# Kernel tuning notes

Hardware: AMD Instinct MI355X
Metric: run time of the kernel (lower is better)

The kernel has to match this reference:

```python
import jax, jax.numpy as jnp
import numpy as np

N_NODES = 100000


def _gcn_conv(x, W, b, row, col, norm, n):
    # PyG GCNConv: h = x @ W, then symmetric-normalized scatter-add, then bias
    h = x @ W                          # [N, out]
    msg = h[col] * norm[:, None]       # gather at source nodes, scale per-edge
    out = jax.ops.segment_sum(msg, row, num_segments=n)  # scatter-add to dest
    return out + b


def setup_inputs() -> dict:
    key = jax.random.key(0)
    k1, k2, k3, k4, k5, k6 = jax.random.split(key, 6)
    F_in, H, C = 128, 128, 64
    E = 1600000
    x = jax.random.normal(k1, (N_NODES, F_in), dtype=jnp.float32)
    edge_index = jax.random.randint(k2, (2, E), 0, N_NODES, dtype=jnp.int64)
    s1 = 1.0 / np.sqrt(F_in)
    s2 = 1.0 / np.sqrt(H)
    W1 = jax.random.uniform(k3, (F_in, H), jnp.float32, -s1, s1)
    b1 = jax.random.uniform(k4, (H,), jnp.float32, -s1, s1)
    W2 = jax.random.uniform(k5, (H, C), jnp.float32, -s2, s2)
    b2 = jax.random.uniform(k6, (C,), jnp.float32, -s2, s2)
    return {"x": x, "edge_index": edge_index, "W1": W1, "b1": b1, "W2": W2, "b2": b2}


def reference(x, edge_index, W1, b1, W2, b2):
    n = x.shape[0]
    # add self-loops (GCNConv default)
    loops = jnp.arange(n, dtype=edge_index.dtype)
    row = jnp.concatenate([edge_index[0], loops])  # destination
    col = jnp.concatenate([edge_index[1], loops])  # source
    # symmetric normalization deg^{-1/2}[row] * deg^{-1/2}[col]
    deg = jax.ops.segment_sum(jnp.ones_like(row, dtype=x.dtype), row, num_segments=n)
    dinv = jnp.where(deg > 0, jax.lax.rsqrt(deg), 0.0)
    norm = dinv[row] * dinv[col]       # [E+N]
    h = jax.nn.relu(_gcn_conv(x, W1, b1, row, col, norm, n))
    # dropout is identity in eval mode
    out = _gcn_conv(h, W2, b2, row, col, norm, n)
    return jax.nn.log_softmax(out, axis=1)
```

## Files before the change

### kernel.cpp

```cpp
#include <hip/hip_runtime.h>
#include <hip/hip_fp16.h>
#include <cstdint>
#include <cstddef>

#define TPB 256
#define CAP 64
#define FWSHIFT 9
#define FWROWS 512
#define CAPB 96
#define DEC_ITERS 32


using half8 = __attribute__((ext_vector_type(8))) _Float16;
using f32x4 = __attribute__((ext_vector_type(4))) float;

__global__ void k_setup(const void* __restrict__ ei, int E, int N,
                        const float* __restrict__ W1, const float* __restrict__ W2,
                        _Float16* __restrict__ wf1, _Float16* __restrict__ wf2,
                        int2* __restrict__ bpairs, int* __restrict__ bcnt,
                        int nDec, int nFW) {
    int b = blockIdx.x;
    if (b < 16) {
        int i = b * TPB + threadIdx.x;
        int k  = i >> 5;
        int n0 = (i & 31) * 4;
        float4 w = ((const float4*)W1)[i];
        int ct = n0 >> 4, kb = k >> 5;
        int lane0 = ((k >> 3) & 3) * 16 + (n0 & 15);
        int j = k & 7;
        int base = ((ct * 4 + kb) * 64 + lane0) * 8 + j;
        wf1[base]      = (_Float16)w.x;
        wf1[base + 8]  = (_Float16)w.y;
        wf1[base + 16] = (_Float16)w.z;
        wf1[base + 24] = (_Float16)w.w;
    } else if (b < 24) {
        int i = (b - 16) * TPB + threadIdx.x;
        int k  = i >> 4;
        int n0 = (i & 15) * 4;
        float4 w = ((const float4*)W2)[i];
        int ct = n0 >> 4, kb = k >> 5;
        int lane0 = ((k >> 3) & 3) * 16 + (n0 & 15);
        int j = k & 7;
        int base = ((ct * 4 + kb) * 64 + lane0) * 8 + j;
        wf2[base]      = (_Float16)w.x;
        wf2[base + 8]  = (_Float16)w.y;
        wf2[base + 16] = (_Float16)w.z;
        wf2[base + 24] = (_Float16)w.w;
    } else {
        const int dblk = b - 24;
        const int tid  = threadIdx.x;
        __shared__ int bad;
        __shared__ int cur[256];
        if (tid == 0) bad = 0;
        for (int f = tid; f < nFW; f += TPB) cur[f] = 0;
        __syncthreads();
        if (tid < 256) {
            long long v = ((const long long*)ei)[tid];
            if (v < 0 || v >= (long long)N) bad = 1;
        }
        __syncthreads();
        const int is64 = !bad;
        const int base = dblk * (TPB * DEC_ITERS);
        const long long* e64 = (const long long*)ei;
        const int* e32 = (const int*)ei;

        for (int it = 0; it < DEC_ITERS; it += 4) {
            int d[4], s[4]; bool val[4];
#pragma unroll
            for (int k = 0; k < 4; ++k) {
                int e = base + (it + k) * TPB + tid;
                val[k] = e < E;
                if (val[k]) {
                    if (is64) { d[k] = (int)e64[e]; s[k] = (int)e64[(long long)E + e]; }
                    else      { d[k] = e32[e];      s[k] = e32[E + e]; }
                }
            }
#pragma unroll
            for (int k = 0; k < 4; ++k) {
                if (val[k]) {
                    int fw  = d[k] >> FWSHIFT;
                    int pos = atomicAdd(&cur[fw], 1);
                    if (pos < CAPB)
                        bpairs[((size_t)fw * nDec + dblk) * CAPB + pos] =
                            make_int2(d[k], s[k]);
                }
            }
        }
        __syncthreads();
        for (int f = tid; f < nFW; f += TPB) {
            int c = cur[f];
            bcnt[(size_t)f * nDec + dblk] = c > CAPB ? CAPB : c;
        }
    }
}

__global__ __launch_bounds__(256)
void k_mega(const int2* __restrict__ bpairs, const int* __restrict__ bcnt,
            int nDec, int N,
            int* __restrict__ cnt, float* __restrict__ dinv,
            int* __restrict__ slots,
            const float* __restrict__ x, const half8* __restrict__ wf1,
            __half* __restrict__ xw1, int nFW, int nGemm) {
    __shared__ __align__(16) _Float16 Of[4][16 * 136];
    __shared__ int cur[FWROWS];
    __shared__ int sc[256];
    __shared__ int excl[257];

    const int tid = threadIdx.x;

    if ((int)blockIdx.x < nFW) {
        const int fw = blockIdx.x;
        for (int i = tid; i < FWROWS; i += TPB) cur[i] = 0;
        int c = (tid < nDec) ? bcnt[(size_t)fw * nDec + tid] : 0;
        sc[tid] = c;
        __syncthreads();
        for (int off = 1; off < 256; off <<= 1) {
            int v = (tid >= off) ? sc[tid - off] : 0;
            __syncthreads();
            sc[tid] += v;
            __syncthreads();
        }
        if (tid == 0) excl[0] = 0;
        excl[tid + 1] = sc[tid];
        __syncthreads();
        const int total = excl[nDec];

        for (int i = tid; i < total; i += TPB) {
            int lo = 0, hi = nDec;
            while (hi - lo > 1) {
                int mid = (lo + hi) >> 1;
                if (excl[mid] <= i) lo = mid; else hi = mid;
            }
            int2 p = bpairs[((size_t)fw * nDec + lo) * CAPB + (i - excl[lo])];
            int pos = atomicAdd(&cur[p.x - (fw << FWSHIFT)], 1);
            if (pos < CAP)
                slots[(size_t)p.x * CAP + pos] = p.y;
        }
        __syncthreads();
        for (int i = tid; i < FWROWS; i += TPB) {
            int node = (fw << FWSHIFT) + i;
            if (node < N) {
                int cc = cur[i];
                cnt[node]  = cc;
                dinv[node] = rsqrtf((float)cc + 1.0f);
            }
        }
    } else {
        const int gb = (int)blockIdx.x - nFW;
        const int wave = tid >> 6, lane = tid & 63;
        const int m = lane & 15, quad = lane >> 4;
        const int nRowTiles = (N + 15) >> 4;

        for (int rt = gb * 4 + wave; rt < nRowTiles; rt += nGemm * 4) {
            const int row0 = rt * 16;
            const int arow = row0 + m;
            const bool rvalid = arow < N;
            const float* xrow = x + (size_t)(rvalid ? arow : 0) * 128;

            f32x4 acc[8];
#pragma unroll
            for (int ct = 0; ct < 8; ++ct) acc[ct] = (f32x4){0.f, 0.f, 0.f, 0.f};

#pragma unroll
            for (int kb = 0; kb < 4; ++kb) {
                const float4* ap = (const float4*)(xrow + kb * 32 + quad * 8);
                float4 a0 = ap[0], a1 = ap[1];
                half8 a;
                a[0] = (_Float16)a0.x; a[1] = (_Float16)a0.y;
                a[2] = (_Float16)a0.z; a[3] = (_Float16)a0.w;
                a[4] = (_Float16)a1.x; a[5] = (_Float16)a1.y;
                a[6] = (_Float16)a1.z; a[7] = (_Float16)a1.w;
#pragma unroll
                for (int ct = 0; ct < 8; ++ct) {
                    half8 bfr = wf1[(ct * 4 + kb) * 64 + lane];
                    acc[ct] = __builtin_amdgcn_mfma_f32_16x16x32_f16(a, bfr, acc[ct], 0, 0, 0);
                }
            }

            _Float16* myO = &Of[wave][0];
#pragma unroll
            for (int ct = 0; ct < 8; ++ct)
#pragma unroll
                for (int r = 0; r < 4; ++r)
                    myO[(quad * 4 + r) * 136 + ct * 16 + m] = (_Float16)acc[ct][r];
            int vr = N - row0; if (vr > 16) vr = 16;
            float4* dst = (float4*)(xw1 + (size_t)row0 * 128);
            for (int i = lane; i < vr * 16; i += 64) {
                int r = i >> 4, q = i & 15;
                dst[r * 16 + q] = *(const float4*)&myO[r * 136 + q * 8];
            }
        }
    }
}

__global__ __launch_bounds__(256)
void k_g1g2(const __half* __restrict__ xw1, const int* __restrict__ cnt,
            const float* __restrict__ dinv,
            const int* __restrict__ slots, const float* __restrict__ bias,
            const half8* __restrict__ wf2, __half* __restrict__ xw2, int N) {
    __shared__ __align__(16) _Float16 Ht[16 * 136];
    __shared__ __align__(16) _Float16 Of[16 * 72];
    __shared__ float dv16[16];

    const int row0 = blockIdx.x * 16;
    const int local = threadIdx.x >> 4;
    const int lane16 = threadIdx.x & 15;
    const int node = row0 + local;

    {
        union { __half2 h2[4]; float4 f; } u;
        float dvn = 0.f;
        if (node < N) {
            int cn = cnt[node];
            int len = cn > CAP ? CAP : cn;
            dvn = dinv[node];
            const int* sl = slots + (size_t)node * CAP;
            float acc[8];
            {
                float4 raw = *(const float4*)(xw1 + (size_t)node * 128 + lane16 * 8);
                const __half2* hp = (const __half2*)&raw;
#pragma unroll
                for (int k = 0; k < 4; ++k) {
                    float2 f = __half22float2(hp[k]);
                    acc[2 * k] = dvn * f.x; acc[2 * k + 1] = dvn * f.y;
                }
            }
            int j = 0;
            for (; j + 3 < len; j += 4) {
                int4 cc = *(const int4*)(sl + j);
                float dv0 = dinv[cc.x];
                float dv1 = dinv[cc.y];
                float dv2 = dinv[cc.z];
                float dv3 = dinv[cc.w];
                float4 raw0 = *(const float4*)(xw1 + (size_t)cc.x * 128 + lane16 * 8);
                float4 raw1 = *(const float4*)(xw1 + (size_t)cc.y * 128 + lane16 * 8);
                float4 raw2 = *(const float4*)(xw1 + (size_t)cc.z * 128 + lane16 * 8);
                float4 raw3 = *(const float4*)(xw1 + (size_t)cc.w * 128 + lane16 * 8);
                const __half2* h0 = (const __half2*)&raw0;
                const __half2* h1 = (const __half2*)&raw1;
                const __half2* h2 = (const __half2*)&raw2;
                const __half2* h3 = (const __half2*)&raw3;
#pragma unroll
                for (int k = 0; k < 4; ++k) {
                    float2 f0 = __half22float2(h0[k]);
                    float2 f1 = __half22float2(h1[k]);
                    float2 f2 = __half22float2(h2[k]);
                    float2 f3 = __half22float2(h3[k]);
                    acc[2 * k]     = fmaf(dv0, f0.x, fmaf(dv1, f1.x,
                                     fmaf(dv2, f2.x, fmaf(dv3, f3.x, acc[2 * k]))));
                    acc[2 * k + 1] = fmaf(dv0, f0.y, fmaf(dv1, f1.y,
                                     fmaf(dv2, f2.y, fmaf(dv3, f3.y, acc[2 * k + 1]))));
                }
            }
            for (; j < len; ++j) {
                int c = sl[j];
                float dv = dinv[c];
                float4 raw = *(const float4*)(xw1 + (size_t)c * 128 + lane16 * 8);
                const __half2* hp = (const __half2*)&raw;
#pragma unroll
                for (int k = 0; k < 4; ++k) {
                    float2 f = __half22float2(hp[k]);
                    acc[2 * k]     = fmaf(dv, f.x, acc[2 * k]);
                    acc[2 * k + 1] = fmaf(dv, f.y, acc[2 * k + 1]);
                }
            }
            float4 b01 = ((const float4*)bias)[lane16 * 2];
            float4 b23 = ((const float4*)bias)[lane16 * 2 + 1];
            float v[8];
            v[0] = b01.x + dvn * acc[0]; v[1] = b01.y + dvn * acc[1];
            v[2] = b01.z + dvn * acc[2]; v[3] = b01.w + dvn * acc[3];
            v[4] = b23.x + dvn * acc[4]; v[5] = b23.y + dvn * acc[5];
            v[6] = b23.z + dvn * acc[6]; v[7] = b23.w + dvn * acc[7];
#pragma unroll
            for (int k = 0; k < 4; ++k)
                u.h2[k] = __floats2half2_rn(fmaxf(v[2 * k], 0.f), fmaxf(v[2 * k + 1], 0.f));
        } else {
            u.f = make_float4(0.f, 0.f, 0.f, 0.f);
        }
        if (lane16 == 0) dv16[local] = dvn;
        *(float4*)(Ht + local * 136 + lane16 * 8) = u.f;
    }
    __syncthreads();

    {
        const int wave = threadIdx.x >> 6, lane = threadIdx.x & 63;
        const int m = lane & 15, quad = lane >> 4;
        f32x4 acc = (f32x4){0.f, 0.f, 0.f, 0.f};
#pragma unroll
        for (int kb = 0; kb < 4; ++kb) {
            half8 a = *(const half8*)(Ht + m * 136 + kb * 32 + quad * 8);
            half8 b = wf2[(wave * 4 + kb) * 64 + lane];
            acc = __builtin_amdgcn_mfma_f32_16x16x32_f16(a, b, acc, 0, 0, 0);
        }
#pragma unroll
        for (int r = 0; r < 4; ++r)
            Of[(quad * 4 + r) * 72 + wave * 16 + m] =
                (_Float16)(acc[r] * dv16[quad * 4 + r]);
    }
    __syncthreads();
    {
        int vr = N - row0; if (vr > 16) vr = 16;
        float4* dst = (float4*)(xw2 + (size_t)row0 * 64);
        for (int i = threadIdx.x; i < vr * 8; i += TPB) {
            int r = i >> 3, q = i & 7;
            dst[r * 8 + q] = *(const float4*)&Of[r * 72 + q * 8];
        }
    }
}

__global__ void k_gather2_lsm(const __half* __restrict__ xws, const int* __restrict__ cnt,
                              const float* __restrict__ dinv,
                              const int* __restrict__ slots,
                              const float* __restrict__ bias, float* __restrict__ out, int N) {
    long long t = (long long)blockIdx.x * TPB + threadIdx.x;
    int node = (int)(t >> 4);
    int lane = (int)(t & 15);
    if (node >= N) return;
    int cn = cnt[node];
    int len = cn > CAP ? CAP : cn;
    float dvn = dinv[node];
    const int* sl = slots + (size_t)node * CAP;
    float a0, a1, a2, a3;
    {
        float2 raw = *(const float2*)(xws + (size_t)node * 64 + lane * 4);
        const __half2* hp = (const __half2*)&raw;
        float2 f0 = __half22float2(hp[0]), f1 = __half22float2(hp[1]);
        a0 = f0.x; a1 = f0.y; a2 = f1.x; a3 = f1.y;
    }
    int j = 0;
    for (; j + 3 < len; j += 4) {
        int4 cc = *(const int4*)(sl + j);
        float2 raw0 = *(const float2*)(xws + (size_t)cc.x * 64 + lane * 4);
        float2 raw1 = *(const float2*)(xws + (size_t)cc.y * 64 + lane * 4);
        float2 raw2 = *(const float2*)(xws + (size_t)cc.z * 64 + lane * 4);
        float2 raw3 = *(const float2*)(xws + (size_t)cc.w * 64 + lane * 4);
        const __half2* h0 = (const __half2*)&raw0;
        const __half2* h1 = (const __half2*)&raw1;
        const __half2* h2 = (const __half2*)&raw2;
        const __half2* h3 = (const __half2*)&raw3;
        float2 f00 = __half22float2(h0[0]), f01 = __half22float2(h0[1]);
        float2 f10 = __half22float2(h1[0]), f11 = __half22float2(h1[1]);
        float2 f20 = __half22float2(h2[0]), f21 = __half22float2(h2[1]);
        float2 f30 = __half22float2(h3[0]), f31 = __half22float2(h3[1]);
        a0 += (f00.x + f10.x) + (f20.x + f30.x);
        a1 += (f00.y + f10.y) + (f20.y + f30.y);
        a2 += (f01.x + f11.x) + (f21.x + f31.x);
        a3 += (f01.y + f11.y) + (f21.y + f31.y);
    }
    for (; j < len; ++j) {
        int c = sl[j];
        float2 raw = *(const float2*)(xws + (size_t)c * 64 + lane * 4);
        const __half2* hp = (const __half2*)&raw;
        float2 f0 = __half22float2(hp[0]), f1 = __half22float2(hp[1]);
        a0 += f0.x; a1 += f0.y; a2 += f1.x; a3 += f1.y;
    }
    float4 bb = ((const float4*)bias)[lane];
    float v0 = bb.x + dvn * a0, v1 = bb.y + dvn * a1;
    float v2 = bb.z + dvn * a2, v3 = bb.w + dvn * a3;

    float m = fmaxf(fmaxf(v0, v1), fmaxf(v2, v3));
#pragma unroll
    for (int off = 1; off < 16; off <<= 1) m = fmaxf(m, __shfl_xor(m, off));
    float s = expf(v0 - m) + expf(v1 - m) + expf(v2 - m) + expf(v3 - m);
#pragma unroll
    for (int off = 1; off < 16; off <<= 1) s += __shfl_xor(s, off);
    float ls = m + logf(s);
    ((float4*)(out + (size_t)node * 64))[lane] =
        make_float4(v0 - ls, v1 - ls, v2 - ls, v3 - ls);
}

extern "C" void kernel_launch(void* const* d_in, const int* in_sizes, int n_in,
                              void* d_out, int out_size, void* d_ws, size_t ws_size,
                              hipStream_t stream) {
    const float* x  = (const float*)d_in[0];
    const void*  ei = d_in[1];
    const float* W1 = (const float*)d_in[2];
    const float* b1 = (const float*)d_in[3];
    const float* W2 = (const float*)d_in[4];
    const float* b2 = (const float*)d_in[5];
    float* out = (float*)d_out;

    const int N = in_sizes[0] / 128;
    const int E = in_sizes[1] / 2;

    const int nFW  = (N + FWROWS - 1) >> FWSHIFT;
    const int nDec = (E + TPB * DEC_ITERS - 1) / (TPB * DEC_ITERS);

    char* base = (char*)d_ws;
    size_t off = 0;
    auto alloc = [&](size_t bytes) { char* p = base + off; off = (off + bytes + 255) & ~(size_t)255; return p; };
    int*      cnt    = (int*)alloc((size_t)N * sizeof(int));
    float*    dinv   = (float*)alloc((size_t)N * sizeof(float));
    _Float16* wf1    = (_Float16*)alloc(128 * 128 * sizeof(_Float16));
    _Float16* wf2    = (_Float16*)alloc(128 * 64 * sizeof(_Float16));
    int*      bcnt   = (int*)alloc((size_t)nFW * nDec * sizeof(int));
    int2*     bpairs = (int2*)alloc((size_t)nFW * nDec * CAPB * sizeof(int2));
    int*      slots  = (int*)alloc((size_t)N * CAP * sizeof(int));
    __half*   xw1    = (__half*)alloc((size_t)N * 128 * sizeof(__half));
    __half*   xw2    = (__half*)alloc((size_t)N * 64 * sizeof(__half));
    (void)ws_size;

    const int nGemm = 512;
    const int nodeTiles = (N + 15) / 16;

    k_setup<<<24 + nDec, TPB, 0, stream>>>(ei, E, N, W1, W2, wf1, wf2,
                                           bpairs, bcnt, nDec, nFW);

    k_mega<<<nFW + nGemm, TPB, 0, stream>>>(bpairs, bcnt, nDec, N, cnt, dinv,
                                            slots, x, (const half8*)wf1, xw1,
                                            nFW, nGemm);

    k_g1g2<<<nodeTiles, TPB, 0, stream>>>(xw1, cnt, dinv, slots, b1,
                                          (const half8*)wf2, xw2, N);

    {
        long long t = (long long)N * 16;
        k_gather2_lsm<<<(int)((t + TPB - 1) / TPB), TPB, 0, stream>>>(xw2, cnt, dinv, slots, b2, out, N);
    }
}
```

Before: 257.7 us.

## Move X@W1 GEMM into setup kernel, split slot fill, unroll gathers by 8

The dense X@W1 GEMM moves out of the mega kernel into the edge-decode setup kernel. Each GEMM block converts W1 into fp16 MFMA fragments in shared memory instead of reading a prepacked global buffer. Slot filling becomes its own kernel that walks each decode bucket sequentially with vector loads, replacing the prefix-scan plus binary-search indexing. Both gather kernels gain an 8-wide unrolled loop to keep more independent loads in flight. The cost is that every GEMM block redoes the W1 conversion, and the setup kernel's shared-memory footprint and register pressure grow.

```diff
diff --git a/kernel.cpp b/kernel.cpp
--- a/kernel.cpp
+++ b/kernel.cpp
@@ -14,27 +14,26 @@
 using half8 = __attribute__((ext_vector_type(8))) _Float16;
 using f32x4 = __attribute__((ext_vector_type(4))) float;
 
-__global__ void k_setup(const void* __restrict__ ei, int E, int N,
-                        const float* __restrict__ W1, const float* __restrict__ W2,
-                        _Float16* __restrict__ wf1, _Float16* __restrict__ wf2,
-                        int2* __restrict__ bpairs, int* __restrict__ bcnt,
-                        int nDec, int nFW) {
-    int b = blockIdx.x;
-    if (b < 16) {
-        int i = b * TPB + threadIdx.x;
-        int k  = i >> 5;
-        int n0 = (i & 31) * 4;
-        float4 w = ((const float4*)W1)[i];
-        int ct = n0 >> 4, kb = k >> 5;
-        int lane0 = ((k >> 3) & 3) * 16 + (n0 & 15);
-        int j = k & 7;
-        int base = ((ct * 4 + kb) * 64 + lane0) * 8 + j;
-        wf1[base]      = (_Float16)w.x;
-        wf1[base + 8]  = (_Float16)w.y;
-        wf1[base + 16] = (_Float16)w.z;
-        wf1[base + 24] = (_Float16)w.w;
-    } else if (b < 24) {
-        int i = (b - 16) * TPB + threadIdx.x;
+struct GemmSm {
+    _Float16 Wl[32 * 64 * 8];
+    _Float16 Of[4][16 * 136];
+};
+struct DecSm { int cur[256]; int bad; };
+union SetupSm { GemmSm g; DecSm d; };
+
+__global__ __launch_bounds__(256)
+void k_setup(const void* __restrict__ ei, int E, int N,
+             const float* __restrict__ W1, const float* __restrict__ W2,
+             _Float16* __restrict__ wf2,
+             int2* __restrict__ bpairs, int* __restrict__ bcnt,
+             int nDec, int nFW,
+             const float* __restrict__ x, __half* __restrict__ xw1, int nGemm) {
+    __shared__ __align__(16) SetupSm sm;
+    const int b = blockIdx.x;
+    const int tid = threadIdx.x;
+
+    if (b < 8) {
+        int i = b * TPB + tid;
         int k  = i >> 4;
         int n0 = (i & 15) * 4;
         float4 w = ((const float4*)W2)[i];
@@ -46,20 +45,17 @@
         wf2[base + 8]  = (_Float16)w.y;
         wf2[base + 16] = (_Float16)w.z;
         wf2[base + 24] = (_Float16)w.w;
-    } else {
-        const int dblk = b - 24;
-        const int tid  = threadIdx.x;
-        __shared__ int bad;
-        __shared__ int cur[256];
-        if (tid == 0) bad = 0;
-        for (int f = tid; f < nFW; f += TPB) cur[f] = 0;
+    } else if (b < 8 + nDec) {
+        const int dblk = b - 8;
+        if (tid == 0) sm.d.bad = 0;
+        for (int f = tid; f < nFW; f += TPB) sm.d.cur[f] = 0;
         __syncthreads();
-        if (tid < 256) {
+        {
             long long v = ((const long long*)ei)[tid];
-            if (v < 0 || v >= (long long)N) bad = 1;
+            if (v < 0 || v >= (long long)N) sm.d.bad = 1;
         }
         __syncthreads();
-        const int is64 = !bad;
+        const int is64 = !sm.d.bad;
         const int base = dblk * (TPB * DEC_ITERS);
         const long long* e64 = (const long long*)ei;
         const int* e32 = (const int*)ei;
@@ -79,7 +75,7 @@
             for (int k = 0; k < 4; ++k) {
                 if (val[k]) {
                     int fw  = d[k] >> FWSHIFT;
-                    int pos = atomicAdd(&cur[fw], 1);
+                    int pos = atomicAdd(&sm.d.cur[fw], 1);
                     if (pos < CAPB)
                         bpairs[((size_t)fw * nDec + dblk) * CAPB + pos] =
                             make_int2(d[k], s[k]);
@@ -88,65 +84,26 @@
         }
         __syncthreads();
         for (int f = tid; f < nFW; f += TPB) {
-            int c = cur[f];
+            int c = sm.d.cur[f];
             bcnt[(size_t)f * nDec + dblk] = c > CAPB ? CAPB : c;
         }
-    }
-}
-
-__global__ __launch_bounds__(256)
-void k_mega(const int2* __restrict__ bpairs, const int* __restrict__ bcnt,
-            int nDec, int N,
-            int* __restrict__ cnt, float* __restrict__ dinv,
-            int* __restrict__ slots,
-            const float* __restrict__ x, const half8* __restrict__ wf1,
-            __half* __restrict__ xw1, int nFW, int nGemm) {
-    __shared__ __align__(16) _Float16 Of[4][16 * 136];
-    __shared__ int cur[FWROWS];
-    __shared__ int sc[256];
-    __shared__ int excl[257];
-
-    const int tid = threadIdx.x;
-
-    if ((int)blockIdx.x < nFW) {
-        const int fw = blockIdx.x;
-        for (int i = tid; i < FWROWS; i += TPB) cur[i] = 0;
-        int c = (tid < nDec) ? bcnt[(size_t)fw * nDec + tid] : 0;
-        sc[tid] = c;
+    } else {
+        const int gb = b - 8 - nDec;
+        for (int i = tid; i < 4096; i += TPB) {
+            float4 w = ((const float4*)W1)[i];
+            int k  = i >> 5;
+            int n0 = (i & 31) * 4;
+            int ct = n0 >> 4, kb = k >> 5;
+            int lane0 = ((k >> 3) & 3) * 16 + (n0 & 15);
+            int j = k & 7;
+            int bs = ((ct * 4 + kb) * 64 + lane0) * 8 + j;
+            sm.g.Wl[bs]      = (_Float16)w.x;
+            sm.g.Wl[bs + 8]  = (_Float16)w.y;
+            sm.g.Wl[bs + 16] = (_Float16)w.z;
+            sm.g.Wl[bs + 24] = (_Float16)w.w;
+        }
         __syncthreads();
-        for (int off = 1; off < 256; off <<= 1) {
-            int v = (tid >= off) ? sc[tid - off] : 0;
-            __syncthreads();
-            sc[tid] += v;
-            __syncthreads();
-        }
-        if (tid == 0) excl[0] = 0;
-        excl[tid + 1] = sc[tid];
-        __syncthreads();
-        const int total = excl[nDec];
-
-        for (int i = tid; i < total; i += TPB) {
-            int lo = 0, hi = nDec;
-            while (hi - lo > 1) {
-                int mid = (lo + hi) >> 1;
-                if (excl[mid] <= i) lo = mid; else hi = mid;
-            }
-            int2 p = bpairs[((size_t)fw * nDec + lo) * CAPB + (i - excl[lo])];
-            int pos = atomicAdd(&cur[p.x - (fw << FWSHIFT)], 1);
-            if (pos < CAP)
-                slots[(size_t)p.x * CAP + pos] = p.y;
-        }
-        __syncthreads();
-        for (int i = tid; i < FWROWS; i += TPB) {
-            int node = (fw << FWSHIFT) + i;
-            if (node < N) {
-                int cc = cur[i];
-                cnt[node]  = cc;
-                dinv[node] = rsqrtf((float)cc + 1.0f);
-            }
-        }
-    } else {
-        const int gb = (int)blockIdx.x - nFW;
+        const half8* wl = (const half8*)sm.g.Wl;
         const int wave = tid >> 6, lane = tid & 63;
         const int m = lane & 15, quad = lane >> 4;
         const int nRowTiles = (N + 15) >> 4;
@@ -172,12 +129,12 @@
                 a[6] = (_Float16)a1.z; a[7] = (_Float16)a1.w;
 #pragma unroll
                 for (int ct = 0; ct < 8; ++ct) {
-                    half8 bfr = wf1[(ct * 4 + kb) * 64 + lane];
+                    half8 bfr = wl[(ct * 4 + kb) * 64 + lane];
                     acc[ct] = __builtin_amdgcn_mfma_f32_16x16x32_f16(a, bfr, acc[ct], 0, 0, 0);
                 }
             }
 
-            _Float16* myO = &Of[wave][0];
+            _Float16* myO = &sm.g.Of[wave][0];
 #pragma unroll
             for (int ct = 0; ct < 8; ++ct)
 #pragma unroll
@@ -189,6 +146,53 @@
                 int r = i >> 4, q = i & 15;
                 dst[r * 16 + q] = *(const float4*)&myO[r * 136 + q * 8];
             }
+        }
+    }
+}
+
+__global__ __launch_bounds__(256)
+void k_fill(const int2* __restrict__ bpairs, const int* __restrict__ bcnt,
+            int nDec, int N,
+            int* __restrict__ cnt, float* __restrict__ dinv,
+            int* __restrict__ slots) {
+    __shared__ int cur[FWROWS];
+    const int fw = blockIdx.x;
+    const int tid = threadIdx.x;
+    const int lo = fw << FWSHIFT;
+    for (int i = tid; i < FWROWS; i += TPB) cur[i] = 0;
+    __syncthreads();
+
+    for (int s = tid; s < nDec; s += TPB) {
+        const int c = bcnt[(size_t)fw * nDec + s];
+        const int2* bp = bpairs + ((size_t)fw * nDec + s) * CAPB;
+        int j = 0;
+        for (; j + 3 < c; j += 4) {
+            const int4* q4 = (const int4*)(bp + j);
+            int4 u0 = q4[0], u1 = q4[1];
+            int2 p0 = make_int2(u0.x, u0.y), p1 = make_int2(u0.z, u0.w);
+            int2 p2 = make_int2(u1.x, u1.y), p3 = make_int2(u1.z, u1.w);
+            int q0 = atomicAdd(&cur[p0.x - lo], 1);
+            int q1 = atomicAdd(&cur[p1.x - lo], 1);
+            int q2 = atomicAdd(&cur[p2.x - lo], 1);
+            int q3 = atomicAdd(&cur[p3.x - lo], 1);
+            if (q0 < CAP) slots[(size_t)p0.x * CAP + q0] = p0.y;
+            if (q1 < CAP) slots[(size_t)p1.x * CAP + q1] = p1.y;
+            if (q2 < CAP) slots[(size_t)p2.x * CAP + q2] = p2.y;
+            if (q3 < CAP) slots[(size_t)p3.x * CAP + q3] = p3.y;
+        }
+        for (; j < c; ++j) {
+            int2 p = bp[j];
+            int pos = atomicAdd(&cur[p.x - lo], 1);
+            if (pos < CAP) slots[(size_t)p.x * CAP + pos] = p.y;
+        }
+    }
+    __syncthreads();
+    for (int i = tid; i < FWROWS; i += TPB) {
+        int node = lo + i;
+        if (node < N) {
+            int cc = cur[i];
+            cnt[node]  = cc;
+            dinv[node] = rsqrtf((float)cc + 1.0f);
         }
     }
 }
@@ -226,20 +230,59 @@
                 }
             }
             int j = 0;
+            for (; j + 7 < len; j += 8) {
+                int4 ca = *(const int4*)(sl + j);
+                int4 cb = *(const int4*)(sl + j + 4);
+                float dv0 = dinv[ca.x], dv1 = dinv[ca.y];
+                float dv2 = dinv[ca.z], dv3 = dinv[ca.w];
+                float dv4 = dinv[cb.x], dv5 = dinv[cb.y];
+                float dv6 = dinv[cb.z], dv7 = dinv[cb.w];
+                float4 r0 = *(const float4*)(xw1 + (size_t)ca.x * 128 + lane16 * 8);
+                float4 r1 = *(const float4*)(xw1 + (size_t)ca.y * 128 + lane16 * 8);
+                float4 r2 = *(const float4*)(xw1 + (size_t)ca.z * 128 + lane16 * 8);
+                float4 r3 = *(const float4*)(xw1 + (size_t)ca.w * 128 + lane16 * 8);
+                float4 r4 = *(const float4*)(xw1 + (size_t)cb.x * 128 + lane16 * 8);
+                float4 r5 = *(const float4*)(xw1 + (size_t)cb.y * 128 + lane16 * 8);
+                float4 r6 = *(const float4*)(xw1 + (size_t)cb.z * 128 + lane16 * 8);
+                float4 r7 = *(const float4*)(xw1 + (size_t)cb.w * 128 + lane16 * 8);
+                const __half2* h0 = (const __half2*)&r0;
+                const __half2* h1 = (const __half2*)&r1;
+                const __half2* h2 = (const __half2*)&r2;
+                const __half2* h3 = (const __half2*)&r3;
+                const __half2* h4 = (const __half2*)&r4;
+                const __half2* h5 = (const __half2*)&r5;
+                const __half2* h6 = (const __half2*)&r6;
+                const __half2* h7 = (const __half2*)&r7;
+#pragma unroll
+                for (int k = 0; k < 4; ++k) {
+                    float2 f0 = __half22float2(h0[k]);
+                    float2 f1 = __half22float2(h1[k]);
+                    float2 f2 = __half22float2(h2[k]);
+                    float2 f3 = __half22float2(h3[k]);
+                    float2 f4 = __half22float2(h4[k]);
+                    float2 f5 = __half22float2(h5[k]);
+                    float2 f6 = __half22float2(h6[k]);
+                    float2 f7 = __half22float2(h7[k]);
+                    float Ax = fmaf(dv0, f0.x, fmaf(dv1, f1.x, fmaf(dv2, f2.x, dv3 * f3.x)));
+                    float Bx = fmaf(dv4, f4.x, fmaf(dv5, f5.x, fmaf(dv6, f6.x, dv7 * f7.x)));
+                    float Ay = fmaf(dv0, f0.y, fmaf(dv1, f1.y, fmaf(dv2, f2.y, dv3 * f3.y)));
+                    float By = fmaf(dv4, f4.y, fmaf(dv5, f5.y, fmaf(dv6, f6.y, dv7 * f7.y)));
+                    acc[2 * k]     += Ax + Bx;
+                    acc[2 * k + 1] += Ay + By;
+                }
+            }
             for (; j + 3 < len; j += 4) {
                 int4 cc = *(const int4*)(sl + j);
-                float dv0 = dinv[cc.x];
-                float dv1 = dinv[cc.y];
-                float dv2 = dinv[cc.z];
-                float dv3 = dinv[cc.w];
-                float4 raw0 = *(const float4*)(xw1 + (size_t)cc.x * 128 + lane16 * 8);
-                float4 raw1 = *(const float4*)(xw1 + (size_t)cc.y * 128 + lane16 * 8);
-                float4 raw2 = *(const float4*)(xw1 + (size_t)cc.z * 128 + lane16 * 8);
-                float4 raw3 = *(const float4*)(xw1 + (size_t)cc.w * 128 + lane16 * 8);
-                const __half2* h0 = (const __half2*)&raw0;
-                const __half2* h1 = (const __half2*)&raw1;
-                const __half2* h2 = (const __half2*)&raw2;
-                const __half2* h3 = (const __half2*)&raw3;
+                float dv0 = dinv[cc.x], dv1 = dinv[cc.y];
+                float dv2 = dinv[cc.z], dv3 = dinv[cc.w];
+                float4 r0 = *(const float4*)(xw1 + (size_t)cc.x * 128 + lane16 * 8);
+                float4 r1 = *(const float4*)(xw1 + (size_t)cc.y * 128 + lane16 * 8);
+                float4 r2 = *(const float4*)(xw1 + (size_t)cc.z * 128 + lane16 * 8);
+                float4 r3 = *(const float4*)(xw1 + (size_t)cc.w * 128 + lane16 * 8);
+                const __half2* h0 = (const __half2*)&r0;
+                const __half2* h1 = (const __half2*)&r1;
+                const __half2* h2 = (const __half2*)&r2;
+                const __half2* h3 = (const __half2*)&r3;
 #pragma unroll
                 for (int k = 0; k < 4; ++k) {
                     float2 f0 = __half22float2(h0[k]);
@@ -328,16 +371,48 @@
         a0 = f0.x; a1 = f0.y; a2 = f1.x; a3 = f1.y;
     }
     int j = 0;
+    for (; j + 7 < len; j += 8) {
+        int4 ca = *(const int4*)(sl + j);
+        int4 cb = *(const int4*)(sl + j + 4);
+        float2 r0 = *(const float2*)(xws + (size_t)ca.x * 64 + lane * 4);
+        float2 r1 = *(const float2*)(xws + (size_t)ca.y * 64 + lane * 4);
+        float2 r2 = *(const float2*)(xws + (size_t)ca.z * 64 + lane * 4);
+        float2 r3 = *(const float2*)(xws + (size_t)ca.w * 64 + lane * 4);
+        float2 r4 = *(const float2*)(xws + (size_t)cb.x * 64 + lane * 4);
+        float2 r5 = *(const float2*)(xws + (size_t)cb.y * 64 + lane * 4);
+        float2 r6 = *(const float2*)(xws + (size_t)cb.z * 64 + lane * 4);
+        float2 r7 = *(const float2*)(xws + (size_t)cb.w * 64 + lane * 4);
+        const __half2* h0 = (const __half2*)&r0;
+        const __half2* h1 = (const __half2*)&r1;
+        const __half2* h2 = (const __half2*)&r2;
+        const __half2* h3 = (const __half2*)&r3;
+        const __half2* h4 = (const __half2*)&r4;
+        const __half2* h5 = (const __half2*)&r5;
+        const __half2* h6 = (const __half2*)&r6;
+        const __half2* h7 = (const __half2*)&r7;
+        float2 f00 = __half22float2(h0[0]), f01 = __half22float2(h0[1]);
+        float2 f10 = __half22float2(h1[0]), f11 = __half22float2(h1[1]);
+        float2 f20 = __half22float2(h2[0]), f21 = __half22float2(h2[1]);
+        float2 f30 = __half22float2(h3[0]), f31 = __half22float2(h3[1]);
+        float2 f40 = __half22float2(h4[0]), f41 = __half22float2(h4[1]);
+        float2 f50 = __half22float2(h5[0]), f51 = __half22float2(h5[1]);
+        float2 f60 = __half22float2(h6[0]), f61 = __half22float2(h6[1]);
+        float2 f70 = __half22float2(h7[0]), f71 = __half22float2(h7[1]);
+        a0 += ((f00.x + f10.x) + (f20.x + f30.x)) + ((f40.x + f50.x) + (f60.x + f70.x));
+        a1 += ((f00.y + f10.y) + (f20.y + f30.y)) + ((f40.y + f50.y) + (f60.y + f70.y));
+        a2 += ((f01.x + f11.x) + (f21.x + f31.x)) + ((f41.x + f51.x) + (f61.x + f71.x));
+        a3 += ((f01.y + f11.y) + (f21.y + f31.y)) + ((f41.y + f51.y) + (f61.y + f71.y));
+    }
     for (; j + 3 < len; j += 4) {
         int4 cc = *(const int4*)(sl + j);
-        float2 raw0 = *(const float2*)(xws + (size_t)cc.x * 64 + lane * 4);
-        float2 raw1 = *(const float2*)(xws + (size_t)cc.y * 64 + lane * 4);
-        float2 raw2 = *(const float2*)(xws + (size_t)cc.z * 64 + lane * 4);
-        float2 raw3 = *(const float2*)(xws + (size_t)cc.w * 64 + lane * 4);
-        const __half2* h0 = (const __half2*)&raw0;
-        const __half2* h1 = (const __half2*)&raw1;
-        const __half2* h2 = (const __half2*)&raw2;
-        const __half2* h3 = (const __half2*)&raw3;
+        float2 r0 = *(const float2*)(xws + (size_t)cc.x * 64 + lane * 4);
+        float2 r1 = *(const float2*)(xws + (size_t)cc.y * 64 + lane * 4);
+        float2 r2 = *(const float2*)(xws + (size_t)cc.z * 64 + lane * 4);
+        float2 r3 = *(const float2*)(xws + (size_t)cc.w * 64 + lane * 4);
+        const __half2* h0 = (const __half2*)&r0;
+        const __half2* h1 = (const __half2*)&r1;
+        const __half2* h2 = (const __half2*)&r2;
+        const __half2* h3 = (const __half2*)&r3;
         float2 f00 = __half22float2(h0[0]), f01 = __half22float2(h0[1]);
         float2 f10 = __half22float2(h1[0]), f11 = __half22float2(h1[1]);
         float2 f20 = __half22float2(h2[0]), f21 = __half22float2(h2[1]);
@@ -385,13 +460,13 @@
 
     const int nFW  = (N + FWROWS - 1) >> FWSHIFT;
     const int nDec = (E + TPB * DEC_ITERS - 1) / (TPB * DEC_ITERS);
+    const int nGemm = 512;
 
     char* base = (char*)d_ws;
     size_t off = 0;
     auto alloc = [&](size_t bytes) { char* p = base + off; off = (off + bytes + 255) & ~(size_t)255; return p; };
     int*      cnt    = (int*)alloc((size_t)N * sizeof(int));
     float*    dinv   = (float*)alloc((size_t)N * sizeof(float));
-    _Float16* wf1    = (_Float16*)alloc(128 * 128 * sizeof(_Float16));
     _Float16* wf2    = (_Float16*)alloc(128 * 64 * sizeof(_Float16));
     int*      bcnt   = (int*)alloc((size_t)nFW * nDec * sizeof(int));
     int2*     bpairs = (int2*)alloc((size_t)nFW * nDec * CAPB * sizeof(int2));
@@ -400,15 +475,13 @@
     __half*   xw2    = (__half*)alloc((size_t)N * 64 * sizeof(__half));
     (void)ws_size;
 
-    const int nGemm = 512;
     const int nodeTiles = (N + 15) / 16;
 
-    k_setup<<<24 + nDec, TPB, 0, stream>>>(ei, E, N, W1, W2, wf1, wf2,
-                                           bpairs, bcnt, nDec, nFW);
-
-    k_mega<<<nFW + nGemm, TPB, 0, stream>>>(bpairs, bcnt, nDec, N, cnt, dinv,
-                                            slots, x, (const half8*)wf1, xw1,
-                                            nFW, nGemm);
+    k_setup<<<8 + nDec + nGemm, TPB, 0, stream>>>(ei, E, N, W1, W2, wf2,
+                                                  bpairs, bcnt, nDec, nFW,
+                                                  x, xw1, nGemm);
+
+    k_fill<<<nFW, TPB, 0, stream>>>(bpairs, bcnt, nDec, N, cnt, dinv, slots);
 
     k_g1g2<<<nodeTiles, TPB, 0, stream>>>(xw1, cnt, dinv, slots, b1,
                                           (const half8*)wf2, xw2, N);
```

Result: no change. 253.2 us (-1.8%).
